# Performance work log

Hardware: AMD Instinct MI355X
Metric: run time of the kernel (lower is better)

## Reference

```python
import jax, jax.numpy as jnp
import numpy as np

TAU_MEM = 20.0
TAU_SYN = 5.0
ALPHA_MEM = float(np.exp(-1.0 / TAU_MEM))
ALPHA_SYN = float(np.exp(-1.0 / TAU_SYN))
CONNECTIVITY = 0.1
SPECTRAL_RADIUS = 0.9


def setup_inputs() -> dict:
    key = jax.random.key(0)
    k1, k2, k3, k4 = jax.random.split(key, 4)
    B, D, N = 2048, 256, 512
    rates = jax.random.normal(k1, (B, D), dtype=jnp.float32)
    input_weight = jax.random.normal(k2, (N, D), dtype=jnp.float32) * 0.1
    W = jax.random.normal(k3, (N, N), dtype=jnp.float32)
    mask = (jax.random.uniform(k4, (N, N)) < CONNECTIVITY).astype(jnp.float32)
    W = W * mask
    # mirror torch init: scale by spectral_radius / max eigvalsh
    max_eig = jnp.linalg.eigvalsh(W)[-1]
    W = W * (SPECTRAL_RADIUS / max_eig)
    return {
        "rates": rates,
        "input_weight": input_weight,
        "reservoir_weight": W,
        "v_mem": jnp.zeros((B, N), dtype=jnp.float32),
        "current": jnp.zeros((B, N), dtype=jnp.float32),
        "n_steps": 64,
    }


def reference(rates, input_weight, reservoir_weight, v_mem, current, n_steps):
    dtype = rates.dtype
    # input current is identical every step in the original loop -> hoist it
    input_current = rates @ input_weight.T  # (B, N)

    def step(carry, _):
        v, c, spike_sum = carry
        rec = (c > 0).astype(dtype) @ reservoir_weight  # (B, N)
        c = ALPHA_SYN * c + (1.0 - ALPHA_SYN) * (input_current + rec)
        v = ALPHA_MEM * v + (1.0 - ALPHA_MEM) * c
        spike_sum = spike_sum + (v > 0).astype(dtype)
        return (v, c, spike_sum), None

    (v, c, spike_sum), _ = jax.lax.scan(
        step, (v_mem, current, jnp.zeros_like(v_mem)), None, length=n_steps
    )
    readout = spike_sum / n_steps  # == stack(spikes).mean(dim=1)
    return readout, (v, c)
```

## Files before the change

### kernel.cpp

```cpp
#include <hip/hip_runtime.h>
#include <stdint.h>


#define N_NEU 512
#define B_ROWS 2048
#define D_IN 256
#define R_PB 8
#define NBLK (B_ROWS / R_PB)

#define WS_PERM    0
#define WS_RANK    2048
#define WS_CNT     4096
#define WS_CNTW    8192
#define WS_IBASE   8256
#define WS_WBASE   8320
#define WS_IDX     16384
#define WS_WT      81920

#define SPK_OFF(k)  ((k) << 3)
#define SPK_REGION  4096

__global__ __launch_bounds__(256) void lsm_count(
    const float* __restrict__ W, uint32_t* __restrict__ ws)
{
    int t  = threadIdx.x;
    int k0 = blockIdx.x * 4;
    int c0 = 0, c1 = 0;
    #pragma unroll
    for (int kk = 0; kk < 4; ++kk) {
        const float* row = W + (size_t)(k0 + kk) * N_NEU;
        c0 += (row[t]       != 0.0f) ? 1 : 0;
        c1 += (row[t + 256] != 0.0f) ? 1 : 0;
    }
    if (c0) atomicAdd(&ws[(WS_CNT >> 2) + t],       (uint32_t)c0);
    if (c1) atomicAdd(&ws[(WS_CNT >> 2) + t + 256], (uint32_t)c1);
}

__global__ __launch_bounds__(512) void lsm_sort(uint32_t* __restrict__ ws)
{
    __shared__ int hist[N_NEU + 1];
    __shared__ int csort[N_NEU];
    __shared__ int gcw[8];

    int t = threadIdx.x;
    int creal = (int)ws[(WS_CNT >> 2) + t];
    for (int i = t; i < N_NEU + 1; i += 512) hist[i] = 0;
    __syncthreads();
    atomicAdd(&hist[creal], 1);
    __syncthreads();
    if (t == 0) {
        int acc = 0;
        for (int v = 0; v <= N_NEU; ++v) { int h = hist[v]; hist[v] = acc; acc += h; }
    }
    __syncthreads();
    int rank = atomicAdd(&hist[creal], 1);
    ws[(WS_PERM >> 2) + rank] = (uint32_t)t;
    ws[(WS_RANK >> 2) + t]    = (uint32_t)rank;
    csort[rank] = creal;
    __syncthreads();
    if (t < 8) {
        int cw = csort[t * 64 + 63];
        cw = (cw + 7) & ~7;
        gcw[t] = cw;
        ws[(WS_CNTW >> 2) + t] = (uint32_t)cw;
    }
    __syncthreads();
    if (t == 0) {
        int ai = 0, aw = 0;
        for (int g = 0; g < 8; ++g) {
            ws[(WS_IBASE >> 2) + g] = (uint32_t)ai;
            ws[(WS_WBASE >> 2) + g] = (uint32_t)aw;
            ai += gcw[g] * 64 * 2;
            aw += gcw[g] * 64 * 4;
        }
    }
    __syncthreads();
    int wg = rank >> 6, ls = rank & 63;
    int cw = gcw[wg];
    uint32_t ib = ws[(WS_IBASE >> 2) + wg];
    uint32_t wb = ws[(WS_WBASE >> 2) + wg];
    char* base = (char*)ws;
    for (int j = creal; j < cw; ++j) {
        *(unsigned short*)(base + WS_IDX + ib + (j >> 3) * 1024 + ls * 16 + (j & 7) * 2) = 0;
        *(float*)(base + WS_WT + wb + (j >> 3) * 2048 + ls * 32 + (j & 7) * 4) = 0.0f;
    }
}

__global__ __launch_bounds__(64) void lsm_fill(
    const float* __restrict__ W, uint32_t* __restrict__ ws)
{
    int c    = blockIdx.x;
    int lane = threadIdx.x;
    char* base = (char*)ws;
    uint32_t rank = ws[(WS_RANK >> 2) + c];
    int wg = (int)(rank >> 6), ls = (int)(rank & 63);
    uint32_t ib = ws[(WS_IBASE >> 2) + wg];
    uint32_t wb = ws[(WS_WBASE >> 2) + wg];

    __shared__ int ctr;
    if (lane == 0) ctr = 0;
    __syncthreads();

    for (int k = lane; k < N_NEU; k += 64) {
        float wv = W[(size_t)k * N_NEU + c];
        if (wv != 0.0f) {
            int j = atomicAdd(&ctr, 1);
            *(unsigned short*)(base + WS_IDX + ib + (j >> 3) * 1024 + ls * 16 + (j & 7) * 2)
                = (unsigned short)SPK_OFF(k);
            *(float*)(base + WS_WT + wb + (j >> 3) * 2048 + ls * 32 + (j & 7) * 4) = wv;
        }
    }
}

#define GATH(P, X) \
    P##0 = *(const uint2*)(smem + ((X).x & 0xffffu)); \
    P##1 = *(const uint2*)(smem + ((X).x >> 16));     \
    P##2 = *(const uint2*)(smem + ((X).y & 0xffffu)); \
    P##3 = *(const uint2*)(smem + ((X).y >> 16));     \
    P##4 = *(const uint2*)(smem + ((X).z & 0xffffu)); \
    P##5 = *(const uint2*)(smem + ((X).z >> 16));     \
    P##6 = *(const uint2*)(smem + ((X).w & 0xffffu)); \
    P##7 = *(const uint2*)(smem + ((X).w >> 16));

#define C1(S, W) \
    rec0 = fmaf((W), (float)((S).x & 0xffu),         rec0); \
    rec1 = fmaf((W), (float)(((S).x >> 8) & 0xffu),  rec1); \
    rec2 = fmaf((W), (float)(((S).x >> 16) & 0xffu), rec2); \
    rec3 = fmaf((W), (float)((S).x >> 24),           rec3); \
    rec4 = fmaf((W), (float)((S).y & 0xffu),         rec4); \
    rec5 = fmaf((W), (float)(((S).y >> 8) & 0xffu),  rec5); \
    rec6 = fmaf((W), (float)(((S).y >> 16) & 0xffu), rec6); \
    rec7 = fmaf((W), (float)((S).y >> 24),           rec7);

#define CONS(P, WA, WB) \
    C1(P##0, (WA).x) C1(P##1, (WA).y) C1(P##2, (WA).z) C1(P##3, (WA).w) \
    C1(P##4, (WB).x) C1(P##5, (WB).y) C1(P##6, (WB).z) C1(P##7, (WB).w)

#define LDW(WA, WB, K) \
    WA = ((const float4*)(wp0 + (K) * 2048))[0]; \
    WB = ((const float4*)(wp0 + (K) * 2048))[1];

__global__ __launch_bounds__(512, 1)
void lsm_main(
    const float* __restrict__ rates, const float* __restrict__ inW,
    const float* __restrict__ vin,   const float* __restrict__ cin,
    const int* __restrict__ nsteps_p,
    const uint32_t* __restrict__ ws, float* __restrict__ out)
{
    __shared__ __align__(16) unsigned char smem[SPK_REGION + 8192];
    float* rl = (float*)(smem + SPK_REGION);

    int q    = threadIdx.x;
    int blk  = blockIdx.x;
    int r0   = blk * R_PB;
    int wg   = q >> 6;
    int lane = q & 63;
    int n    = (int)ws[(WS_PERM >> 2) + q];
    int cw   = (int)ws[(WS_CNTW >> 2) + wg];
    int nit  = cw >> 3;
    const char* ip0 = (const char*)ws + WS_IDX + ws[(WS_IBASE >> 2) + wg]
                    + lane * 16;
    const char* wp0 = (const char*)ws + WS_WT  + ws[(WS_WBASE >> 2) + wg]
                    + lane * 32;
    int spk_n = SPK_OFF(n);

    ((float4*)rl)[q] = ((const float4*)(rates + (size_t)r0 * D_IN))[q];
    __syncthreads();

    float I[R_PB] = {0.f, 0.f, 0.f, 0.f, 0.f, 0.f, 0.f, 0.f};
    {
        const float4* wrow = (const float4*)(inW + (size_t)n * D_IN);
        for (int d4 = 0; d4 < D_IN / 4; ++d4) {
            float4 wv = wrow[d4];
            #pragma unroll
            for (int r = 0; r < R_PB; ++r) {
                const float* rr = rl + r * D_IN + d4 * 4;
                I[r] += wv.x * rr[0] + wv.y * rr[1] + wv.z * rr[2] + wv.w * rr[3];
            }
        }
    }

    float c0v[R_PB], v0v[R_PB], ssum[R_PB];
    uint2 sini = make_uint2(0u, 0u);
    #pragma unroll
    for (int r = 0; r < R_PB; ++r) {
        c0v[r] = cin[(size_t)(r0 + r) * N_NEU + n];
        v0v[r] = vin[(size_t)(r0 + r) * N_NEU + n];
        ssum[r] = 0.f;
        unsigned bit = (c0v[r] > 0.f) ? 1u : 0u;
        if (r < 4) sini.x |= bit << (r * 8);
        else       sini.y |= bit << ((r - 4) * 8);
    }
    *(uint2*)(smem + spk_n) = sini;

    uint4 xr0, xr1, xr2, xr3, xr4, xr5, xr6, xr7, xr8, xr9, xr10, xr11;
    const uint4 xz = make_uint4(0u, 0u, 0u, 0u);
    xr0  =              *(const uint4*)(ip0);
    xr1  = (1  < nit) ? *(const uint4*)(ip0 + 1024)  : xz;
    xr2  = (2  < nit) ? *(const uint4*)(ip0 + 2048)  : xz;
    xr3  = (3  < nit) ? *(const uint4*)(ip0 + 3072)  : xz;
    xr4  = (4  < nit) ? *(const uint4*)(ip0 + 4096)  : xz;
    xr5  = (5  < nit) ? *(const uint4*)(ip0 + 5120)  : xz;
    xr6  = (6  < nit) ? *(const uint4*)(ip0 + 6144)  : xz;
    xr7  = (7  < nit) ? *(const uint4*)(ip0 + 7168)  : xz;
    xr8  = (8  < nit) ? *(const uint4*)(ip0 + 8192)  : xz;
    xr9  = (9  < nit) ? *(const uint4*)(ip0 + 9216)  : xz;
    xr10 = (10 < nit) ? *(const uint4*)(ip0 + 10240) : xz;
    xr11 = (11 < nit) ? *(const uint4*)(ip0 + 11264) : xz;

    const float AS   = (float)0.8187307530779818;
    const float OMAS = (float)(1.0 - 0.8187307530779818);
    const float AM   = (float)0.9512294245007140;
    const float OMAM = (float)(1.0 - 0.9512294245007140);

    int T = nsteps_p[0];
    __syncthreads();

    #pragma unroll 1
    for (int t = 0; t < T; ++t) {
        float rec0 = 0.f, rec1 = 0.f, rec2 = 0.f, rec3 = 0.f;
        float rec4 = 0.f, rec5 = 0.f, rec6 = 0.f, rec7 = 0.f;
        uint2 a0, a1, a2, a3, a4, a5, a6, a7;
        uint2 b0, b1, b2, b3, b4, b5, b6, b7;
        float4 waA, wbA, waB, wbB;

        LDW(waA, wbA, 0)
        GATH(a, xr0)
        if (1 < nit)  { LDW(waB, wbB, 1)  GATH(b, xr1)  }
        CONS(a, waA, wbA)
        if (1 < nit)  {
            if (2 < nit)  { LDW(waA, wbA, 2)  GATH(a, xr2)  }
            CONS(b, waB, wbB)
        }
        if (2 < nit)  {
            if (3 < nit)  { LDW(waB, wbB, 3)  GATH(b, xr3)  }
            CONS(a, waA, wbA)
        }
        if (3 < nit)  {
            if (4 < nit)  { LDW(waA, wbA, 4)  GATH(a, xr4)  }
            CONS(b, waB, wbB)
        }
        if (4 < nit)  {
            if (5 < nit)  { LDW(waB, wbB, 5)  GATH(b, xr5)  }
            CONS(a, waA, wbA)
        }
        if (5 < nit)  {
            if (6 < nit)  { LDW(waA, wbA, 6)  GATH(a, xr6)  }
            CONS(b, waB, wbB)
        }
        if (6 < nit)  {
            if (7 < nit)  { LDW(waB, wbB, 7)  GATH(b, xr7)  }
            CONS(a, waA, wbA)
        }
        if (7 < nit)  {
            if (8 < nit)  { LDW(waA, wbA, 8)  GATH(a, xr8)  }
            CONS(b, waB, wbB)
        }
        if (8 < nit)  {
            if (9 < nit)  { LDW(waB, wbB, 9)  GATH(b, xr9)  }
            CONS(a, waA, wbA)
        }
        if (9 < nit)  {
            if (10 < nit) { LDW(waA, wbA, 10) GATH(a, xr10) }
            CONS(b, waB, wbB)
        }
        if (10 < nit) {
            if (11 < nit) { LDW(waB, wbB, 11) GATH(b, xr11) }
            CONS(a, waA, wbA)
        }
        if (11 < nit) {
            CONS(b, waB, wbB)
        }

        __syncthreads();

        uint2 ns = make_uint2(0u, 0u);
        {
            float rca[R_PB] = {rec0, rec1, rec2, rec3, rec4, rec5, rec6, rec7};
            #pragma unroll
            for (int r = 0; r < R_PB; ++r) {
                c0v[r] = AS * c0v[r] + OMAS * (I[r] + rca[r]);
                v0v[r] = AM * v0v[r] + OMAM * c0v[r];
                ssum[r] += (v0v[r] > 0.f) ? 1.f : 0.f;
                unsigned bit = (c0v[r] > 0.f) ? 1u : 0u;
                if (r < 4) ns.x |= bit << (r * 8);
                else       ns.y |= bit << ((r - 4) * 8);
            }
        }
        *(uint2*)(smem + spk_n) = ns;
        __syncthreads();
    }

    float invT = 1.0f / (float)T;
    size_t BN = (size_t)B_ROWS * N_NEU;
    #pragma unroll
    for (int r = 0; r < R_PB; ++r) {
        size_t off = (size_t)(r0 + r) * N_NEU + n;
        out[off]          = ssum[r] * invT;
        out[BN + off]     = v0v[r];
        out[2 * BN + off] = c0v[r];
    }
}

extern "C" void kernel_launch(void* const* d_in, const int* in_sizes, int n_in,
                              void* d_out, int out_size, void* d_ws, size_t ws_size,
                              hipStream_t stream)
{
    const float* rates = (const float*)d_in[0];
    const float* inW   = (const float*)d_in[1];
    const float* W     = (const float*)d_in[2];
    const float* vin   = (const float*)d_in[3];
    const float* cin   = (const float*)d_in[4];
    const int*   nst   = (const int*)d_in[5];
    uint32_t* ws = (uint32_t*)d_ws;
    float* out = (float*)d_out;
    (void)in_sizes; (void)n_in; (void)out_size; (void)ws_size;

    hipMemsetAsync((char*)d_ws + WS_CNT, 0, 2048, stream);

    lsm_count<<<128, 256, 0, stream>>>(W, ws);
    lsm_sort<<<1, 512, 0, stream>>>(ws);
    lsm_fill<<<N_NEU, 64, 0, stream>>>(W, ws);
    lsm_main<<<NBLK, 512, 0, stream>>>(rates, inW, vin, cin, nst, ws, out);
}
```

Measured before the change: 363.5 us.

## Halve rows per block to run two blocks per CU and balance wave loads

Each block now handles 4 batch rows instead of 8. That doubles the block count, and launch bounds allow two resident blocks per CU. Spike bits pack into one 32-bit word per neuron, so each gather loads one dword instead of a uint2, and half the rec accumulators are dropped. Waves 4-7 now take wavegroups in reversed order, which pairs heavy and light sparse columns on each SIMD. The cost is that each gathered weight is reused across fewer rows, so per-step weight and index traffic from cache roughly doubles overall.

New measurement: 427.6 us. 17.6% more time.

```diff
diff --git a/kernel.cpp b/kernel.cpp
--- a/kernel.cpp
+++ b/kernel.cpp
@@ -5,7 +5,7 @@
 #define N_NEU 512
 #define B_ROWS 2048
 #define D_IN 256
-#define R_PB 8
+#define R_PB 4
 #define NBLK (B_ROWS / R_PB)
 
 #define WS_PERM    0
@@ -17,8 +17,8 @@
 #define WS_IDX     16384
 #define WS_WT      81920
 
-#define SPK_OFF(k)  ((k) << 3)
-#define SPK_REGION  4096
+#define SPK_OFF(k)  ((k) << 2)
+#define SPK_REGION  2048
 
 __global__ __launch_bounds__(256) void lsm_count(
     const float* __restrict__ W, uint32_t* __restrict__ ws)
@@ -113,24 +113,20 @@
 }
 
 #define GATH(P, X) \
-    P##0 = *(const uint2*)(smem + ((X).x & 0xffffu)); \
-    P##1 = *(const uint2*)(smem + ((X).x >> 16));     \
-    P##2 = *(const uint2*)(smem + ((X).y & 0xffffu)); \
-    P##3 = *(const uint2*)(smem + ((X).y >> 16));     \
-    P##4 = *(const uint2*)(smem + ((X).z & 0xffffu)); \
-    P##5 = *(const uint2*)(smem + ((X).z >> 16));     \
-    P##6 = *(const uint2*)(smem + ((X).w & 0xffffu)); \
-    P##7 = *(const uint2*)(smem + ((X).w >> 16));
+    P##0 = *(const unsigned*)(smem + ((X).x & 0xffffu)); \
+    P##1 = *(const unsigned*)(smem + ((X).x >> 16));     \
+    P##2 = *(const unsigned*)(smem + ((X).y & 0xffffu)); \
+    P##3 = *(const unsigned*)(smem + ((X).y >> 16));     \
+    P##4 = *(const unsigned*)(smem + ((X).z & 0xffffu)); \
+    P##5 = *(const unsigned*)(smem + ((X).z >> 16));     \
+    P##6 = *(const unsigned*)(smem + ((X).w & 0xffffu)); \
+    P##7 = *(const unsigned*)(smem + ((X).w >> 16));
 
 #define C1(S, W) \
-    rec0 = fmaf((W), (float)((S).x & 0xffu),         rec0); \
-    rec1 = fmaf((W), (float)(((S).x >> 8) & 0xffu),  rec1); \
-    rec2 = fmaf((W), (float)(((S).x >> 16) & 0xffu), rec2); \
-    rec3 = fmaf((W), (float)((S).x >> 24),           rec3); \
-    rec4 = fmaf((W), (float)((S).y & 0xffu),         rec4); \
-    rec5 = fmaf((W), (float)(((S).y >> 8) & 0xffu),  rec5); \
-    rec6 = fmaf((W), (float)(((S).y >> 16) & 0xffu), rec6); \
-    rec7 = fmaf((W), (float)((S).y >> 24),           rec7);
+    rec0 = fmaf((W), (float)((S) & 0xffu),         rec0); \
+    rec1 = fmaf((W), (float)(((S) >> 8) & 0xffu),  rec1); \
+    rec2 = fmaf((W), (float)(((S) >> 16) & 0xffu), rec2); \
+    rec3 = fmaf((W), (float)((S) >> 24),           rec3);
 
 #define CONS(P, WA, WB) \
     C1(P##0, (WA).x) C1(P##1, (WA).y) C1(P##2, (WA).z) C1(P##3, (WA).w) \
@@ -140,22 +136,24 @@
     WA = ((const float4*)(wp0 + (K) * 2048))[0]; \
     WB = ((const float4*)(wp0 + (K) * 2048))[1];
 
-__global__ __launch_bounds__(512, 1)
+__global__ __launch_bounds__(512, 2)
 void lsm_main(
     const float* __restrict__ rates, const float* __restrict__ inW,
     const float* __restrict__ vin,   const float* __restrict__ cin,
     const int* __restrict__ nsteps_p,
     const uint32_t* __restrict__ ws, float* __restrict__ out)
 {
-    __shared__ __align__(16) unsigned char smem[SPK_REGION + 8192];
+    __shared__ __align__(16) unsigned char smem[SPK_REGION + 4096];
     float* rl = (float*)(smem + SPK_REGION);
 
     int q    = threadIdx.x;
     int blk  = blockIdx.x;
     int r0   = blk * R_PB;
-    int wg   = q >> 6;
+    int w    = q >> 6;
     int lane = q & 63;
-    int n    = (int)ws[(WS_PERM >> 2) + q];
+    int wg   = (w < 4) ? w : (11 - w);
+    int rslot = wg * 64 + lane;
+    int n    = (int)ws[(WS_PERM >> 2) + rslot];
     int cw   = (int)ws[(WS_CNTW >> 2) + wg];
     int nit  = cw >> 3;
     const char* ip0 = (const char*)ws + WS_IDX + ws[(WS_IBASE >> 2) + wg]
@@ -164,10 +162,11 @@
                     + lane * 32;
     int spk_n = SPK_OFF(n);
 
-    ((float4*)rl)[q] = ((const float4*)(rates + (size_t)r0 * D_IN))[q];
-    __syncthreads();
-
-    float I[R_PB] = {0.f, 0.f, 0.f, 0.f, 0.f, 0.f, 0.f, 0.f};
+    if (q < 256)
+        ((float4*)rl)[q] = ((const float4*)(rates + (size_t)r0 * D_IN))[q];
+    __syncthreads();
+
+    float I[R_PB] = {0.f, 0.f, 0.f, 0.f};
     {
         const float4* wrow = (const float4*)(inW + (size_t)n * D_IN);
         for (int d4 = 0; d4 < D_IN / 4; ++d4) {
@@ -181,17 +180,15 @@
     }
 
     float c0v[R_PB], v0v[R_PB], ssum[R_PB];
-    uint2 sini = make_uint2(0u, 0u);
+    unsigned sini = 0u;
     #pragma unroll
     for (int r = 0; r < R_PB; ++r) {
         c0v[r] = cin[(size_t)(r0 + r) * N_NEU + n];
         v0v[r] = vin[(size_t)(r0 + r) * N_NEU + n];
         ssum[r] = 0.f;
-        unsigned bit = (c0v[r] > 0.f) ? 1u : 0u;
-        if (r < 4) sini.x |= bit << (r * 8);
-        else       sini.y |= bit << ((r - 4) * 8);
-    }
-    *(uint2*)(smem + spk_n) = sini;
+        sini |= ((c0v[r] > 0.f) ? 1u : 0u) << (r * 8);
+    }
+    *(unsigned*)(smem + spk_n) = sini;
 
     uint4 xr0, xr1, xr2, xr3, xr4, xr5, xr6, xr7, xr8, xr9, xr10, xr11;
     const uint4 xz = make_uint4(0u, 0u, 0u, 0u);
@@ -219,9 +216,8 @@
     #pragma unroll 1
     for (int t = 0; t < T; ++t) {
         float rec0 = 0.f, rec1 = 0.f, rec2 = 0.f, rec3 = 0.f;
-        float rec4 = 0.f, rec5 = 0.f, rec6 = 0.f, rec7 = 0.f;
-        uint2 a0, a1, a2, a3, a4, a5, a6, a7;
-        uint2 b0, b1, b2, b3, b4, b5, b6, b7;
+        unsigned a0, a1, a2, a3, a4, a5, a6, a7;
+        unsigned b0, b1, b2, b3, b4, b5, b6, b7;
         float4 waA, wbA, waB, wbB;
 
         LDW(waA, wbA, 0)
@@ -274,20 +270,18 @@
 
         __syncthreads();
 
-        uint2 ns = make_uint2(0u, 0u);
+        unsigned ns = 0u;
         {
-            float rca[R_PB] = {rec0, rec1, rec2, rec3, rec4, rec5, rec6, rec7};
+            float rca[R_PB] = {rec0, rec1, rec2, rec3};
             #pragma unroll
             for (int r = 0; r < R_PB; ++r) {
                 c0v[r] = AS * c0v[r] + OMAS * (I[r] + rca[r]);
                 v0v[r] = AM * v0v[r] + OMAM * c0v[r];
                 ssum[r] += (v0v[r] > 0.f) ? 1.f : 0.f;
-                unsigned bit = (c0v[r] > 0.f) ? 1u : 0u;
-                if (r < 4) ns.x |= bit << (r * 8);
-                else       ns.y |= bit << ((r - 4) * 8);
+                ns |= ((c0v[r] > 0.f) ? 1u : 0u) << (r * 8);
             }
         }
-        *(uint2*)(smem + spk_n) = ns;
+        *(unsigned*)(smem + spk_n) = ns;
         __syncthreads();
     }
 
```

## Double-buffer spike array, drop one barrier, preload first weight chunks, balance wave mapping

Applied to the files above, without the earlier changes.

The spike bitmap in shared memory now alternates between two buffers, so each step reads the previous buffer and writes the next. That removes the barrier that separated the gather phase from the spike-write phase. The first three weight chunks are kept in registers across all steps to cut per-step global loads. Waves are also remapped (w<4 ? w : 11-w) to interleave heavy and light neuron groups, which costs extra register pressure in exchange.

Measured after the change: 366.7 us. About the same (+0.9%).

```diff
diff --git a/kernel.cpp b/kernel.cpp
--- a/kernel.cpp
+++ b/kernel.cpp
@@ -18,7 +18,7 @@
 #define WS_WT      81920
 
 #define SPK_OFF(k)  ((k) << 3)
-#define SPK_REGION  4096
+#define SPK_BUF     4096
 
 __global__ __launch_bounds__(256) void lsm_count(
     const float* __restrict__ W, uint32_t* __restrict__ ws)
@@ -112,15 +112,15 @@
     }
 }
 
-#define GATH(P, X) \
-    P##0 = *(const uint2*)(smem + ((X).x & 0xffffu)); \
-    P##1 = *(const uint2*)(smem + ((X).x >> 16));     \
-    P##2 = *(const uint2*)(smem + ((X).y & 0xffffu)); \
-    P##3 = *(const uint2*)(smem + ((X).y >> 16));     \
-    P##4 = *(const uint2*)(smem + ((X).z & 0xffffu)); \
-    P##5 = *(const uint2*)(smem + ((X).z >> 16));     \
-    P##6 = *(const uint2*)(smem + ((X).w & 0xffffu)); \
-    P##7 = *(const uint2*)(smem + ((X).w >> 16));
+#define GATH(P, X, B) \
+    P##0 = *(const uint2*)((B) + ((X).x & 0xffffu)); \
+    P##1 = *(const uint2*)((B) + ((X).x >> 16));     \
+    P##2 = *(const uint2*)((B) + ((X).y & 0xffffu)); \
+    P##3 = *(const uint2*)((B) + ((X).y >> 16));     \
+    P##4 = *(const uint2*)((B) + ((X).z & 0xffffu)); \
+    P##5 = *(const uint2*)((B) + ((X).z >> 16));     \
+    P##6 = *(const uint2*)((B) + ((X).w & 0xffffu)); \
+    P##7 = *(const uint2*)((B) + ((X).w >> 16));
 
 #define C1(S, W) \
     rec0 = fmaf((W), (float)((S).x & 0xffu),         rec0); \
@@ -147,15 +147,16 @@
     const int* __restrict__ nsteps_p,
     const uint32_t* __restrict__ ws, float* __restrict__ out)
 {
-    __shared__ __align__(16) unsigned char smem[SPK_REGION + 8192];
-    float* rl = (float*)(smem + SPK_REGION);
+    __shared__ __align__(16) unsigned char smem[2 * SPK_BUF + 8192];
+    float* rl = (float*)(smem + 2 * SPK_BUF);
 
     int q    = threadIdx.x;
     int blk  = blockIdx.x;
     int r0   = blk * R_PB;
-    int wg   = q >> 6;
+    int w    = q >> 6;
     int lane = q & 63;
-    int n    = (int)ws[(WS_PERM >> 2) + q];
+    int wg   = (w < 4) ? w : (11 - w);
+    int n    = (int)ws[(WS_PERM >> 2) + wg * 64 + lane];
     int cw   = (int)ws[(WS_CNTW >> 2) + wg];
     int nit  = cw >> 3;
     const char* ip0 = (const char*)ws + WS_IDX + ws[(WS_IBASE >> 2) + wg]
@@ -208,6 +209,15 @@
     xr10 = (10 < nit) ? *(const uint4*)(ip0 + 10240) : xz;
     xr11 = (11 < nit) ? *(const uint4*)(ip0 + 11264) : xz;
 
+    float4 rw0a, rw0b, rw1a, rw1b, rw2a, rw2b;
+    const float4 fz = make_float4(0.f, 0.f, 0.f, 0.f);
+    rw0a = ((const float4*)wp0)[0];
+    rw0b = ((const float4*)wp0)[1];
+    rw1a = (1 < nit) ? ((const float4*)(wp0 + 2048))[0] : fz;
+    rw1b = (1 < nit) ? ((const float4*)(wp0 + 2048))[1] : fz;
+    rw2a = (2 < nit) ? ((const float4*)(wp0 + 4096))[0] : fz;
+    rw2b = (2 < nit) ? ((const float4*)(wp0 + 4096))[1] : fz;
+
     const float AS   = (float)0.8187307530779818;
     const float OMAS = (float)(1.0 - 0.8187307530779818);
     const float AM   = (float)0.9512294245007140;
@@ -218,61 +228,62 @@
 
     #pragma unroll 1
     for (int t = 0; t < T; ++t) {
+        const unsigned char* sb = smem + ((t & 1) ? SPK_BUF : 0);
+        unsigned char*       db = smem + ((t & 1) ? 0 : SPK_BUF);
+
         float rec0 = 0.f, rec1 = 0.f, rec2 = 0.f, rec3 = 0.f;
         float rec4 = 0.f, rec5 = 0.f, rec6 = 0.f, rec7 = 0.f;
         uint2 a0, a1, a2, a3, a4, a5, a6, a7;
         uint2 b0, b1, b2, b3, b4, b5, b6, b7;
         float4 waA, wbA, waB, wbB;
 
-        LDW(waA, wbA, 0)
-        GATH(a, xr0)
-        if (1 < nit)  { LDW(waB, wbB, 1)  GATH(b, xr1)  }
-        CONS(a, waA, wbA)
-        if (1 < nit)  {
-            if (2 < nit)  { LDW(waA, wbA, 2)  GATH(a, xr2)  }
-            CONS(b, waB, wbB)
-        }
-        if (2 < nit)  {
-            if (3 < nit)  { LDW(waB, wbB, 3)  GATH(b, xr3)  }
+        GATH(a, xr0, sb)
+        if (3 < nit) { LDW(waB, wbB, 3) }
+        if (1 < nit) { GATH(b, xr1, sb) }
+        CONS(a, rw0a, rw0b)
+        if (1 < nit) {
+            if (2 < nit) { GATH(a, xr2, sb) }
+            CONS(b, rw1a, rw1b)
+        }
+        if (2 < nit) {
+            if (3 < nit) { GATH(b, xr3, sb) }
+            CONS(a, rw2a, rw2b)
+        }
+        if (3 < nit) {
+            if (4 < nit)  { LDW(waA, wbA, 4)  GATH(a, xr4, sb)  }
+            CONS(b, waB, wbB)
+        }
+        if (4 < nit) {
+            if (5 < nit)  { LDW(waB, wbB, 5)  GATH(b, xr5, sb)  }
             CONS(a, waA, wbA)
         }
-        if (3 < nit)  {
-            if (4 < nit)  { LDW(waA, wbA, 4)  GATH(a, xr4)  }
-            CONS(b, waB, wbB)
-        }
-        if (4 < nit)  {
-            if (5 < nit)  { LDW(waB, wbB, 5)  GATH(b, xr5)  }
+        if (5 < nit) {
+            if (6 < nit)  { LDW(waA, wbA, 6)  GATH(a, xr6, sb)  }
+            CONS(b, waB, wbB)
+        }
+        if (6 < nit) {
+            if (7 < nit)  { LDW(waB, wbB, 7)  GATH(b, xr7, sb)  }
             CONS(a, waA, wbA)
         }
-        if (5 < nit)  {
-            if (6 < nit)  { LDW(waA, wbA, 6)  GATH(a, xr6)  }
-            CONS(b, waB, wbB)
-        }
-        if (6 < nit)  {
-            if (7 < nit)  { LDW(waB, wbB, 7)  GATH(b, xr7)  }
+        if (7 < nit) {
+            if (8 < nit)  { LDW(waA, wbA, 8)  GATH(a, xr8, sb)  }
+            CONS(b, waB, wbB)
+        }
+        if (8 < nit) {
+            if (9 < nit)  { LDW(waB, wbB, 9)  GATH(b, xr9, sb)  }
             CONS(a, waA, wbA)
         }
-        if (7 < nit)  {
-            if (8 < nit)  { LDW(waA, wbA, 8)  GATH(a, xr8)  }
-            CONS(b, waB, wbB)
-        }
-        if (8 < nit)  {
-            if (9 < nit)  { LDW(waB, wbB, 9)  GATH(b, xr9)  }
+        if (9 < nit) {
+            if (10 < nit) { LDW(waA, wbA, 10) GATH(a, xr10, sb) }
+            CONS(b, waB, wbB)
+        }
+        if (10 < nit) {
+            if (11 < nit) { LDW(waB, wbB, 11) GATH(b, xr11, sb) }
             CONS(a, waA, wbA)
         }
-        if (9 < nit)  {
-            if (10 < nit) { LDW(waA, wbA, 10) GATH(a, xr10) }
-            CONS(b, waB, wbB)
-        }
-        if (10 < nit) {
-            if (11 < nit) { LDW(waB, wbB, 11) GATH(b, xr11) }
-            CONS(a, waA, wbA)
-        }
         if (11 < nit) {
             CONS(b, waB, wbB)
         }
-
-        __syncthreads();
 
         uint2 ns = make_uint2(0u, 0u);
         {
@@ -287,7 +298,7 @@
                 else       ns.y |= bit << ((r - 4) * 8);
             }
         }
-        *(uint2*)(smem + spk_n) = ns;
+        *(uint2*)(db + spk_n) = ns;
         __syncthreads();
     }
 
```
